# Optimization experiments

Measured on AMD Instinct MI355X. Metric: run time of the kernel, lower is better.

The kernel has to match this reference:

```python
import jax, jax.numpy as jnp
import numpy as np

B, C, H, W = 2, 256, 48, 48
NH = 4          # heads (and SE ratio)
DK = C // NH    # 64


def conv1x1(x, w, b):
    # x: [B,Cin,H,W], w: [Cout,Cin], b: [Cout]
    return jnp.einsum('oc,bchw->bohw', w, x) + b[None, :, None, None]


def rtrans(q_in, k_in, v_in, qw, qb, kw, kb, vw, vb):
    b, c, h_, w_ = q_in.shape
    n = h_ * w_
    q = conv1x1(q_in, qw, qb).reshape(b, NH, DK, n).transpose(0, 1, 3, 2)  # [B,h,N,dk]
    k = conv1x1(k_in, kw, kb).reshape(b, NH, DK, n)                         # [B,h,dk,N]
    v = conv1x1(v_in, vw, vb).reshape(b, NH, DK, n)                         # [B,h,dk,N]
    scores = jnp.einsum('bhnd,bhdm->bhnm', q, k) / jnp.sqrt(jnp.asarray(DK, q.dtype))
    attn = jax.nn.softmax(scores, axis=-1)                                  # [B,h,N,N]
    out = jnp.einsum('bhdn,bhnm->bhdm', v, attn)                            # [B,h,dk,N]
    return out.reshape(b, c, h_, w_)


def setup_inputs() -> dict:
    key = jax.random.key(0)
    ks = jax.random.split(key, 16)
    s = 0.02
    d = {
        'x': jax.random.normal(ks[0], (B, C, H, W), jnp.float32),
        'y': jax.random.normal(ks[1], (B, C, H, W), jnp.float32),
        # RScaling: fc1 Conv2d(2C, C//ratio, 1), fc2 Conv2d(C//ratio, 2C, 1); ratio=NH
        'sc_fc1_w': jax.random.normal(ks[2], (C // NH, 2 * C), jnp.float32) * s,
        'sc_fc1_b': jnp.zeros((C // NH,), jnp.float32),
        'sc_fc2_w': jax.random.normal(ks[3], (2 * C, C // NH), jnp.float32) * s,
        'sc_fc2_b': jnp.zeros((2 * C,), jnp.float32),
        # RTrans 1
        't1_qw': jax.random.normal(ks[4], (C, C), jnp.float32) * s,
        't1_qb': jnp.zeros((C,), jnp.float32),
        't1_kw': jax.random.normal(ks[5], (C, C), jnp.float32) * s,
        't1_kb': jnp.zeros((C,), jnp.float32),
        't1_vw': jax.random.normal(ks[6], (C, C), jnp.float32) * s,
        't1_vb': jnp.zeros((C,), jnp.float32),
        # RTrans 2 (ST=True)
        't2_qw': jax.random.normal(ks[7], (C, C), jnp.float32) * s,
        't2_qb': jnp.zeros((C,), jnp.float32),
        't2_kw': jax.random.normal(ks[8], (C, C), jnp.float32) * s,
        't2_kb': jnp.zeros((C,), jnp.float32),
        't2_vw': jax.random.normal(ks[9], (C, C), jnp.float32) * s,
        't2_vb': jnp.zeros((C,), jnp.float32),
        # RGating: Conv2d(2C, 2, 1)
        'gate_w': jax.random.normal(ks[10], (2, 2 * C), jnp.float32) * s,
        'gate_b': jnp.zeros((2,), jnp.float32),
    }
    return d


def reference(x, y, sc_fc1_w, sc_fc1_b, sc_fc2_w, sc_fc2_b,
              t1_qw, t1_qb, t1_kw, t1_kb, t1_vw, t1_vb,
              t2_qw, t2_qb, t2_kw, t2_kb, t2_vw, t2_vb,
              gate_w, gate_b):
    c = x.shape[1]
    # --- RScaling (SE squeeze-excite on concatenated streams) ---
    cat = jnp.concatenate([x, y], axis=1)                       # [B,2C,H,W]
    pooled = cat.mean(axis=(2, 3), keepdims=True)               # [B,2C,1,1]
    f = conv1x1(jax.nn.relu(conv1x1(pooled, sc_fc1_w, sc_fc1_b)), sc_fc2_w, sc_fc2_b)
    g = jax.nn.sigmoid(f)                                       # [B,2C,1,1]
    x = x * g[:, :c] + x
    y = y * g[:, c:] + y
    # --- RTrans 1: x = attn(q=x, k=y, v=y) ---
    x = rtrans(x, y, y, t1_qw, t1_qb, t1_kw, t1_kb, t1_vw, t1_vb)
    # --- RTrans 2 (ST): y = attn(q=y, k=x_new, v=x_new) ---
    y = rtrans(y, x, x, t2_qw, t2_qb, t2_kw, t2_kb, t2_vw, t2_vb)
    # --- RGating ---
    gate = jax.nn.sigmoid(conv1x1(jnp.concatenate([x, y], axis=1), gate_w, gate_b))  # [B,2,H,W]
    x = x * gate[:, :1] + x
    y = y * gate[:, 1:] + y
    return (x, y)
```

## Files before the change

kernel.cpp:

```cpp
#include <hip/hip_runtime.h>
#include <hip/hip_bf16.h>
#include <math.h>

typedef __hip_bfloat16 bf16;
typedef unsigned short u16;
typedef __attribute__((ext_vector_type(8))) short short8;
typedef __attribute__((ext_vector_type(4))) float f32x4;

#define BB  2
#define CC  256
#define NHH 4
#define DKK 64
#define NN  2304
#define NT  36
#define NT2 18
#define MS  4
#define NTM 9
#define WSTR 88
#define MFMA16(a,b,c) __builtin_amdgcn_mfma_f32_16x16x32_bf16(a, b, c, 0, 0, 0)

__device__ __forceinline__ float u2f(u16 u){ return __uint_as_float(((unsigned)u) << 16); }
__device__ __forceinline__ u16 f2u(float f){
    unsigned u = __float_as_uint(f);
    unsigned r = u + 0x7FFFu + ((u >> 16) & 1u);
    return (u16)(r >> 16);
}

__device__ __forceinline__ float ldv(const void* p, size_t i, int bf){
    return bf ? u2f(((const u16*)p)[i]) : ((const float*)p)[i];
}
__device__ __forceinline__ void stv(void* p, size_t i, float v, int bf){
    if (bf) ((u16*)p)[i] = f2u(v);
    else    ((float*)p)[i] = v;
}
__device__ __forceinline__ short8 ldw8(const void* p, size_t i, int bf){
    if (bf) return *(const short8*)((const u16*)p + i);
    const float* f = (const float*)p + i;
    short8 r;
    #pragma unroll
    for (int k = 0; k < 8; k++) r[k] = (short)f2u(f[k]);
    return r;
}

__global__ void detect_kernel(const void* __restrict__ x, int* __restrict__ flg){
    const u16* u = (const u16*)x;
    int t = threadIdx.x;
    bool ok = true;
    for (int i = 0; i < 8; i++){
        u16 v = u[t*8 + i];
        int e = (v >> 7) & 0xFF;
        ok = ok && (((v & 0x7FFF) == 0) || (e >= 96 && e <= 143));
    }
    unsigned long long b = __ballot(ok);
    if (t == 0) *flg = (b == 0xFFFFFFFFFFFFFFFFull) ? 1 : 0;
}

__global__ void pool_kernel(const void* __restrict__ x, const void* __restrict__ y,
                            const int* __restrict__ flg, float* __restrict__ pooled){
    int bf = *flg;
    int bid = blockIdx.x;
    int b = bid >> 9, cc = bid & 511;
    const void* src = (cc < CC) ? x : y;
    size_t base = ((size_t)b*CC + (cc & 255))*NN;
    float s = 0.f;
    for (int i = threadIdx.x; i < NN; i += 256) s += ldv(src, base + i, bf);
    __shared__ float red[4];
    for (int off = 32; off; off >>= 1) s += __shfl_down(s, off, 64);
    if ((threadIdx.x & 63) == 0) red[threadIdx.x >> 6] = s;
    __syncthreads();
    if (threadIdx.x == 0)
        pooled[bid] = (red[0]+red[1]+red[2]+red[3]) * (1.0f/(float)NN);
}

__global__ void se_fc1_kernel(const float* __restrict__ pooled,
                              const void* __restrict__ w1, const void* __restrict__ b1,
                              const int* __restrict__ flg, float* __restrict__ f1){
    int bf = *flg;
    int bid = blockIdx.x;
    int b = bid >> 6, f = bid & 63;
    int lane = threadIdx.x;
    const float* ps = pooled + b*512;
    float a = 0.f;
    #pragma unroll
    for (int k = 0; k < 8; k++){
        int c = lane*8 + k;
        a += ldv(w1, (size_t)f*512 + c, bf) * ps[c];
    }
    #pragma unroll
    for (int off = 32; off; off >>= 1) a += __shfl_down(a, off, 64);
    if (lane == 0)
        f1[b*64 + f] = fmaxf(a + ldv(b1, f, bf), 0.f);
}

__launch_bounds__(512)
__global__ void se_fc2_kernel(const float* __restrict__ f1,
                              const void* __restrict__ w2, const void* __restrict__ b2v,
                              const int* __restrict__ flg, float* __restrict__ gse){
    int bf = *flg;
    int b = blockIdx.x;
    int o = threadIdx.x;
    __shared__ float f1s[64];
    if (o < 64) f1s[o] = f1[b*64 + o];
    __syncthreads();
    float a = ldv(b2v, o, bf);
    #pragma unroll
    for (int j = 0; j < 64; j++) a += ldv(w2, (size_t)o*64 + j, bf) * f1s[j];
    gse[b*512 + o] = 1.f + 1.f/(1.f + __expf(-a));
}

__global__ void transpose2_kernel(const void* __restrict__ x, const void* __restrict__ y,
                                  const float* __restrict__ gse, const int* __restrict__ flg,
                                  u16* __restrict__ xsT, u16* __restrict__ ysT){
    int bf = *flg;
    int z = blockIdx.z;
    int b = z >> 1, which = z & 1;
    const void* src = which ? y : x;
    const float* gs = gse + b*512 + (which ? 256 : 0);
    u16* dst = which ? ysT : xsT;
    int ct = blockIdx.y, nt = blockIdx.x;
    int t = threadIdx.x;
    int nl = t & 63, cq = t >> 6;
    #pragma unroll
    for (int i = 0; i < 16; i++){
        int c = ct*64 + cq*16 + i;
        float v = ldv(src, ((size_t)b*CC + c)*NN + nt*64 + nl, bf) * gs[c];
        dst[((size_t)b*NN + nt*64 + nl)*CC + c] = f2u(v);
    }
}

__launch_bounds__(256)
__global__ void conv3_mfma(const u16* __restrict__ Xq, const u16* __restrict__ Xkv,
                           const void* __restrict__ wq, const void* __restrict__ bq,
                           const void* __restrict__ wk, const void* __restrict__ bk,
                           const void* __restrict__ wv, const void* __restrict__ bv_,
                           const int* __restrict__ flg,
                           u16* __restrict__ QT, u16* __restrict__ KT, u16* __restrict__ Vb){
    int bf = *flg;
    int z = blockIdx.z;
    int b = z / 3, op = z % 3;
    const u16* X = (op == 0) ? Xq : Xkv;
    const void* W    = (op == 0) ? wq : (op == 1) ? wk : wv;
    const void* bias = (op == 0) ? bq : (op == 1) ? bk : bv_;
    u16* Y = (op == 0) ? QT : (op == 1) ? KT : Vb;
    int transT = (op < 2);
    float oscale = (op == 1) ? 0.125f : 1.0f;
    int ot = blockIdx.y, nt = blockIdx.x;
    int lane = threadIdx.x & 63, wv_ = threadIdx.x >> 6;
    int c15 = lane & 15, quad = lane >> 4;
    const u16* Xb = X + ((size_t)b*NN + nt*64)*CC;
    int oa = ot*64 + wv_*16 + c15;
    f32x4 zf = {0.f,0.f,0.f,0.f};
    f32x4 acc[4] = {zf,zf,zf,zf};
    #pragma unroll
    for (int kc = 0; kc < CC; kc += 32){
        short8 aw = ldw8(W, (size_t)oa*CC + kc + quad*8, bf);
        #pragma unroll
        for (int j = 0; j < 4; j++){
            short8 bx = *(const short8*)(Xb + (size_t)(j*16 + c15)*CC + kc + quad*8);
            acc[j] = MFMA16(aw, bx, acc[j]);
        }
    }
    int od = ot*64 + wv_*16 + quad*4;
    float bvr[4];
    #pragma unroll
    for (int r = 0; r < 4; r++) bvr[r] = ldv(bias, od + r, bf);
    #pragma unroll
    for (int j = 0; j < 4; j++){
        int n = nt*64 + j*16 + c15;
        #pragma unroll
        for (int r = 0; r < 4; r++){
            int o = od + r;
            float val = (acc[j][r] + bvr[r]) * oscale;
            size_t idx = transT
              ? (((size_t)(b*NHH + (o >> 6))*NN + n)*DKK + (o & 63))
              : (((size_t)b*CC + o)*NN + n);
            Y[idx] = f2u(val);
        }
    }
}

__launch_bounds__(256)
__global__ void attn_stats_mfma(const u16* __restrict__ QT, const u16* __restrict__ KT,
                                float* __restrict__ gL){
    int bh = blockIdx.y, ntile = blockIdx.x, ms = blockIdx.z;
    int lane = threadIdx.x & 63, wv = threadIdx.x >> 6;
    int c15 = lane & 15, quad = lane >> 4;
    const u16* Qb = QT + (size_t)bh*NN*DKK;
    const u16* Kb = KT + (size_t)bh*NN*DKK;
    size_t qo = (size_t)(ntile*64 + wv*16 + c15)*DKK + quad*8;
    short8 a0 = *(const short8*)(Qb + qo);
    short8 a1 = *(const short8*)(Qb + qo + 32);
    float ll[4] = {0.f,0.f,0.f,0.f};
    f32x4 z = {0.f,0.f,0.f,0.f};
    for (int it = 0; it < NTM; it++){
        int mt = ms*NTM + it;
        f32x4 s[4];
        #pragma unroll
        for (int j = 0; j < 4; j++){
            size_t ko = (size_t)(mt*64 + j*16 + c15)*DKK + quad*8;
            short8 b0 = *(const short8*)(Kb + ko);
            short8 b1 = *(const short8*)(Kb + ko + 32);
            f32x4 t = MFMA16(a0, b0, z);
            s[j]     = MFMA16(a1, b1, t);
        }
        #pragma unroll
        for (int r = 0; r < 4; r++)
            ll[r] += __expf(s[0][r]) + __expf(s[1][r]) + __expf(s[2][r]) + __expf(s[3][r]);
    }
    #pragma unroll
    for (int d = 1; d < 16; d <<= 1)
        #pragma unroll
        for (int r = 0; r < 4; r++)
            ll[r] += __shfl_xor(ll[r], d, 16);
    if (c15 == 0){
        #pragma unroll
        for (int r = 0; r < 4; r++){
            int n = ntile*64 + wv*16 + quad*4 + r;
            gL[((size_t)ms*BB*NHH + bh)*NN + n] = ll[r];
        }
    }
}

__global__ void stats_combine(const float* __restrict__ gL, float* __restrict__ Li){
    int idx = blockIdx.x*256 + threadIdx.x;
    if (idx >= BB*NHH*NN) return;
    float ll = 0.f;
    #pragma unroll
    for (int ms = 0; ms < MS; ms++)
        ll += gL[(size_t)ms*BB*NHH*NN + idx];
    Li[idx] = 1.f/ll;
}

__launch_bounds__(512)
__global__ void attn_out_mfma(const u16* __restrict__ QT, const u16* __restrict__ KT,
                              const u16* __restrict__ V, const float* __restrict__ Li,
                              const int* __restrict__ flg,
                              void* __restrict__ O, size_t ooff, u16* __restrict__ OT){
    int bf = *flg;
    int bh = blockIdx.y, mtile = blockIdx.x;
    int tid = threadIdx.x;
    int lane = tid & 63, wv5 = tid >> 6;
    int g = wv5 >> 2, wv = wv5 & 3;
    int c15 = lane & 15, quad = lane >> 4;
    const u16* Qb = QT + (size_t)bh*NN*DKK;
    const u16* Kb = KT + (size_t)bh*NN*DKK;
    const u16* Vb = V + (size_t)bh*DKK*NN;
    const float* Lp = Li + (size_t)bh*NN;
    __shared__ __align__(16) u16 wT[2][2][64][WSTR];
    __shared__ __align__(16) float osum[64][66];
    short8 kb0[4], kb1[4];
    #pragma unroll
    for (int j = 0; j < 4; j++){
        size_t ko = (size_t)(mtile*64 + j*16 + c15)*DKK + quad*8;
        kb0[j] = *(const short8*)(Kb + ko);
        kb1[j] = *(const short8*)(Kb + ko + 32);
    }
    f32x4 z = {0.f,0.f,0.f,0.f};
    f32x4 o4[4] = {z,z,z,z};
    int nt0 = g*NT2;
    size_t qo0 = (size_t)(nt0*64 + wv*16 + c15)*DKK + quad*8;
    short8 a0 = *(const short8*)(Qb + qo0);
    short8 a1 = *(const short8*)(Qb + qo0 + 32);
    size_t vo0 = (size_t)(wv*16 + c15)*NN + nt0*64 + quad*8;
    short8 av0 = *(const short8*)(Vb + vo0);
    short8 av1 = *(const short8*)(Vb + vo0 + 32);
    for (int it = 0; it < NT2; it++){
        int nt = g*NT2 + it;
        int p = it & 1;
        f32x4 s[4];
        #pragma unroll
        for (int j = 0; j < 4; j++){
            f32x4 t = MFMA16(a0, kb0[j], z);
            s[j]    = MFMA16(a1, kb1[j], t);
        }
        short8 a0n = a0, a1n = a1, av0n = av0, av1n = av1;
        if (it + 1 < NT2){
            size_t qn = (size_t)((nt+1)*64 + wv*16 + c15)*DKK + quad*8;
            a0n = *(const short8*)(Qb + qn);
            a1n = *(const short8*)(Qb + qn + 32);
            size_t vn = (size_t)(wv*16 + c15)*NN + (nt+1)*64 + quad*8;
            av0n = *(const short8*)(Vb + vn);
            av1n = *(const short8*)(Vb + vn + 32);
        }
        int nb = nt*64 + wv*16 + quad*4;
        float iL[4];
        #pragma unroll
        for (int r = 0; r < 4; r++) iL[r] = Lp[nb+r];
        #pragma unroll
        for (int j = 0; j < 4; j++){
            ushort4 pk;
            pk.x = f2u(__expf(s[j][0]) * iL[0]);
            pk.y = f2u(__expf(s[j][1]) * iL[1]);
            pk.z = f2u(__expf(s[j][2]) * iL[2]);
            pk.w = f2u(__expf(s[j][3]) * iL[3]);
            *(ushort4*)&wT[g][p][j*16 + c15][wv*16 + quad*4] = pk;
        }
        __syncthreads();
        #pragma unroll
        for (int j = 0; j < 4; j++){
            short8 b0 = *(const short8*)&wT[g][p][j*16 + c15][quad*8];
            short8 b1 = *(const short8*)&wT[g][p][j*16 + c15][32 + quad*8];
            o4[j] = MFMA16(av0, b0, o4[j]);
            o4[j] = MFMA16(av1, b1, o4[j]);
        }
        a0 = a0n; a1 = a1n; av0 = av0n; av1 = av1n;
    }
    if (g == 1){
        #pragma unroll
        for (int j = 0; j < 4; j++)
            #pragma unroll
            for (int r = 0; r < 4; r++)
                osum[wv*16 + quad*4 + r][j*16 + c15] = o4[j][r];
    }
    __syncthreads();
    if (g == 0){
        int brow = bh >> 2, head = bh & 3;
        #pragma unroll
        for (int j = 0; j < 4; j++){
            int m = mtile*64 + j*16 + c15;
            #pragma unroll
            for (int r = 0; r < 4; r++){
                int d = wv*16 + quad*4 + r;
                float val = o4[j][r] + osum[d][j*16 + c15];
                stv(O, ooff + ((size_t)brow*CC + head*DKK + d)*NN + m, val, bf);
                if (OT) OT[((size_t)brow*NN + m)*CC + head*DKK + d] = f2u(val);
            }
        }
    }
}

__global__ void gate_part_kernel(const void* __restrict__ out, const void* __restrict__ gw,
                                 const int* __restrict__ flg, float* __restrict__ gpart){
    int bf = *flg;
    const size_t SZ = (size_t)BB*CC*NN;
    int b = blockIdx.z, g = blockIdx.y;
    int nb = blockIdx.x*64;
    int t = threadIdx.x;
    int nl = t & 63, sub = t >> 6;
    __shared__ float r0[4][64], r1[4][64];
    float a0 = 0.f, a1 = 0.f;
    int cbase = g*128 + sub*32;
    for (int i = 0; i < 32; i++){
        int cc = cbase + i;
        size_t idx = (cc < 256 ? ((size_t)b*CC + cc)*NN
                               : SZ + ((size_t)b*CC + (cc-256))*NN) + nb + nl;
        float v = ldv(out, idx, bf);
        a0 += ldv(gw, cc, bf)*v;
        a1 += ldv(gw, 512 + cc, bf)*v;
    }
    r0[sub][nl] = a0; r1[sub][nl] = a1;
    __syncthreads();
    if (t < 64){
        float s0 = r0[0][t]+r0[1][t]+r0[2][t]+r0[3][t];
        float s1 = r1[0][t]+r1[1][t]+r1[2][t]+r1[3][t];
        int n = nb + t;
        gpart[(((size_t)b*4 + g)*2 + 0)*NN + n] = s0;
        gpart[(((size_t)b*4 + g)*2 + 1)*NN + n] = s1;
    }
}

__global__ void gate_combine_kernel(const float* __restrict__ gpart, const void* __restrict__ gb,
                                    const int* __restrict__ flg, float* __restrict__ gates){
    int bf = *flg;
    int idx = blockIdx.x*256 + threadIdx.x;
    if (idx >= BB*NN) return;
    int b = idx / NN, n = idx % NN;
    float s0 = ldv(gb, 0, bf), s1 = ldv(gb, 1, bf);
    #pragma unroll
    for (int g = 0; g < 4; g++){
        s0 += gpart[(((size_t)b*4 + g)*2 + 0)*NN + n];
        s1 += gpart[(((size_t)b*4 + g)*2 + 1)*NN + n];
    }
    gates[((size_t)b*2 + 0)*NN + n] = 1.f + 1.f/(1.f + __expf(-s0));
    gates[((size_t)b*2 + 1)*NN + n] = 1.f + 1.f/(1.f + __expf(-s1));
}

__global__ void rescale_kernel(const float* __restrict__ gates, const int* __restrict__ flg,
                               void* __restrict__ out){
    int bf = *flg;
    const size_t SZ = (size_t)BB*CC*NN;
    const size_t nq = (2*SZ) >> 2;
    for (size_t u = (size_t)blockIdx.x*256 + threadIdx.x; u < nq; u += (size_t)gridDim.x*256){
        size_t flat = u*4;
        int half = (int)(flat / SZ);
        size_t rem = flat % SZ;
        int b = (int)(rem / ((size_t)CC*NN));
        int n = (int)(rem % NN);
        const float* gp = gates + ((size_t)b*2 + half)*NN + n;
        #pragma unroll
        for (int k = 0; k < 4; k++)
            stv(out, flat + k, ldv(out, flat + k, bf) * gp[k], bf);
    }
}

extern "C" void kernel_launch(void* const* d_in, const int* in_sizes, int n_in,
                              void* d_out, int out_size, void* d_ws, size_t ws_size,
                              hipStream_t stream){
    (void)in_sizes; (void)n_in; (void)out_size; (void)ws_size;
    const void* x    = d_in[0];
    const void* y    = d_in[1];
    const void* sc1w = d_in[2];
    const void* sc1b = d_in[3];
    const void* sc2w = d_in[4];
    const void* sc2b = d_in[5];
    const void *t1qw = d_in[6],  *t1qb = d_in[7];
    const void *t1kw = d_in[8],  *t1kb = d_in[9];
    const void *t1vw = d_in[10], *t1vb = d_in[11];
    const void *t2qw = d_in[12], *t2qb = d_in[13];
    const void *t2kw = d_in[14], *t2kb = d_in[15];
    const void *t2vw = d_in[16], *t2vb = d_in[17];
    const void *gw   = d_in[18], *gb   = d_in[19];

    const size_t SZ = (size_t)BB*CC*NN;
    const size_t BHN = (size_t)BB*NHH*NN;
    char* wsb = (char*)d_ws;
    int*   flg    = (int*)wsb;
    float* pooled = (float*)(wsb + 16);
    float* f1     = pooled + 1024;
    float* gse    = f1 + 128;
    float* Lb     = gse + 1024;
    float* gL     = Lb + BHN;
    float* gpart  = gL + MS*BHN;
    float* gates  = gpart + (size_t)BB*4*2*NN;
    u16* xsT = (u16*)(gates + (size_t)BB*2*NN);
    u16* ysT = xsT + SZ;
    u16* QT  = ysT + SZ;
    u16* KT  = QT + SZ;
    u16* Vb  = KT + SZ;

    dim3 tg2(NT, 4, BB*2);
    dim3 cg3(NT, 4, BB*3);
    dim3 sg(NT, BB*NHH, MS);
    dim3 ag(NT, BB*NHH);
    dim3 gg(NT, 4, BB);

    detect_kernel<<<1, 64, 0, stream>>>(x, flg);
    pool_kernel<<<1024, 256, 0, stream>>>(x, y, flg, pooled);
    se_fc1_kernel<<<BB*64, 64, 0, stream>>>(pooled, sc1w, sc1b, flg, f1);
    se_fc2_kernel<<<BB, 512, 0, stream>>>(f1, sc2w, sc2b, flg, gse);

    transpose2_kernel<<<tg2, 256, 0, stream>>>(x, y, gse, flg, xsT, ysT);

    conv3_mfma<<<cg3, 256, 0, stream>>>(xsT, ysT, t1qw, t1qb, t1kw, t1kb, t1vw, t1vb,
                                        flg, QT, KT, Vb);
    attn_stats_mfma<<<sg, 256, 0, stream>>>(QT, KT, gL);
    stats_combine<<<72, 256, 0, stream>>>(gL, Lb);
    attn_out_mfma<<<ag, 512, 0, stream>>>(QT, KT, Vb, Lb, flg, d_out, 0, xsT);

    conv3_mfma<<<cg3, 256, 0, stream>>>(ysT, xsT, t2qw, t2qb, t2kw, t2kb, t2vw, t2vb,
                                        flg, QT, KT, Vb);
    attn_stats_mfma<<<sg, 256, 0, stream>>>(QT, KT, gL);
    stats_combine<<<72, 256, 0, stream>>>(gL, Lb);
    attn_out_mfma<<<ag, 512, 0, stream>>>(QT, KT, Vb, Lb, flg, d_out, SZ, (u16*)nullptr);

    gate_part_kernel<<<gg, 256, 0, stream>>>(d_out, gw, flg, gpart);
    gate_combine_kernel<<<18, 256, 0, stream>>>(gpart, gb, flg, gates);
    rescale_kernel<<<1024, 256, 0, stream>>>(gates, flg, d_out);
}
```

Baseline: 402.7 us.

## Flatten grids for XCD-local head mapping and halve attn_out m-tile

The conv, stats and attention-output kernels now use 1D grids. The batch-head (or batch/out-tile) index sits in the low 3 bits of blockIdx.x, so round-robin dispatch across the 8 XCDs keeps each head's Q/K/V traffic within one XCD's L2. The attention-output kernel also shrinks its key/column tile from 64 to 32. That doubles the block count from 288 to 576 to fill more CUs and cuts LDS per block. The cost is that Q and V tiles are reloaded, and QK^T plus exp are recomputed, for twice as many tiles.

After: 428.1 us. 6.3% more time.

```diff
diff --git a/kernel.cpp b/kernel.cpp
--- a/kernel.cpp
+++ b/kernel.cpp
@@ -136,15 +136,16 @@
                            const int* __restrict__ flg,
                            u16* __restrict__ QT, u16* __restrict__ KT, u16* __restrict__ Vb){
     int bf = *flg;
-    int z = blockIdx.z;
-    int b = z / 3, op = z % 3;
+    int bhD = blockIdx.x & 7;
+    int q = blockIdx.x >> 3;
+    int op = q / 36, nt = q % 36;
+    int b = bhD >> 2, ot = bhD & 3;
     const u16* X = (op == 0) ? Xq : Xkv;
     const void* W    = (op == 0) ? wq : (op == 1) ? wk : wv;
     const void* bias = (op == 0) ? bq : (op == 1) ? bk : bv_;
     u16* Y = (op == 0) ? QT : (op == 1) ? KT : Vb;
     int transT = (op < 2);
     float oscale = (op == 1) ? 0.125f : 1.0f;
-    int ot = blockIdx.y, nt = blockIdx.x;
     int lane = threadIdx.x & 63, wv_ = threadIdx.x >> 6;
     int c15 = lane & 15, quad = lane >> 4;
     const u16* Xb = X + ((size_t)b*NN + nt*64)*CC;
@@ -182,7 +183,9 @@
 __launch_bounds__(256)
 __global__ void attn_stats_mfma(const u16* __restrict__ QT, const u16* __restrict__ KT,
                                 float* __restrict__ gL){
-    int bh = blockIdx.y, ntile = blockIdx.x, ms = blockIdx.z;
+    int bh = blockIdx.x & 7;
+    int r2 = blockIdx.x >> 3;
+    int ntile = r2 % 36, ms = r2 / 36;
     int lane = threadIdx.x & 63, wv = threadIdx.x >> 6;
     int c15 = lane & 15, quad = lane >> 4;
     const u16* Qb = QT + (size_t)bh*NN*DKK;
@@ -237,7 +240,8 @@
                               const int* __restrict__ flg,
                               void* __restrict__ O, size_t ooff, u16* __restrict__ OT){
     int bf = *flg;
-    int bh = blockIdx.y, mtile = blockIdx.x;
+    int bh = blockIdx.x & 7;
+    int mtile = blockIdx.x >> 3;
     int tid = threadIdx.x;
     int lane = tid & 63, wv5 = tid >> 6;
     int g = wv5 >> 2, wv = wv5 & 3;
@@ -246,17 +250,17 @@
     const u16* Kb = KT + (size_t)bh*NN*DKK;
     const u16* Vb = V + (size_t)bh*DKK*NN;
     const float* Lp = Li + (size_t)bh*NN;
-    __shared__ __align__(16) u16 wT[2][2][64][WSTR];
-    __shared__ __align__(16) float osum[64][66];
-    short8 kb0[4], kb1[4];
-    #pragma unroll
-    for (int j = 0; j < 4; j++){
-        size_t ko = (size_t)(mtile*64 + j*16 + c15)*DKK + quad*8;
+    __shared__ __align__(16) u16 wT[2][2][32][WSTR];
+    __shared__ __align__(16) float osum[64][34];
+    short8 kb0[2], kb1[2];
+    #pragma unroll
+    for (int j = 0; j < 2; j++){
+        size_t ko = (size_t)(mtile*32 + j*16 + c15)*DKK + quad*8;
         kb0[j] = *(const short8*)(Kb + ko);
         kb1[j] = *(const short8*)(Kb + ko + 32);
     }
     f32x4 z = {0.f,0.f,0.f,0.f};
-    f32x4 o4[4] = {z,z,z,z};
+    f32x4 o4[2] = {z,z};
     int nt0 = g*NT2;
     size_t qo0 = (size_t)(nt0*64 + wv*16 + c15)*DKK + quad*8;
     short8 a0 = *(const short8*)(Qb + qo0);
@@ -267,9 +271,9 @@
     for (int it = 0; it < NT2; it++){
         int nt = g*NT2 + it;
         int p = it & 1;
-        f32x4 s[4];
-        #pragma unroll
-        for (int j = 0; j < 4; j++){
+        f32x4 s[2];
+        #pragma unroll
+        for (int j = 0; j < 2; j++){
             f32x4 t = MFMA16(a0, kb0[j], z);
             s[j]    = MFMA16(a1, kb1[j], t);
         }
@@ -287,7 +291,7 @@
         #pragma unroll
         for (int r = 0; r < 4; r++) iL[r] = Lp[nb+r];
         #pragma unroll
-        for (int j = 0; j < 4; j++){
+        for (int j = 0; j < 2; j++){
             ushort4 pk;
             pk.x = f2u(__expf(s[j][0]) * iL[0]);
             pk.y = f2u(__expf(s[j][1]) * iL[1]);
@@ -297,7 +301,7 @@
         }
         __syncthreads();
         #pragma unroll
-        for (int j = 0; j < 4; j++){
+        for (int j = 0; j < 2; j++){
             short8 b0 = *(const short8*)&wT[g][p][j*16 + c15][quad*8];
             short8 b1 = *(const short8*)&wT[g][p][j*16 + c15][32 + quad*8];
             o4[j] = MFMA16(av0, b0, o4[j]);
@@ -307,7 +311,7 @@
     }
     if (g == 1){
         #pragma unroll
-        for (int j = 0; j < 4; j++)
+        for (int j = 0; j < 2; j++)
             #pragma unroll
             for (int r = 0; r < 4; r++)
                 osum[wv*16 + quad*4 + r][j*16 + c15] = o4[j][r];
@@ -316,8 +320,8 @@
     if (g == 0){
         int brow = bh >> 2, head = bh & 3;
         #pragma unroll
-        for (int j = 0; j < 4; j++){
-            int m = mtile*64 + j*16 + c15;
+        for (int j = 0; j < 2; j++){
+            int m = mtile*32 + j*16 + c15;
             #pragma unroll
             for (int r = 0; r < 4; r++){
                 int d = wv*16 + quad*4 + r;
@@ -429,9 +433,6 @@
     u16* Vb  = KT + SZ;
 
     dim3 tg2(NT, 4, BB*2);
-    dim3 cg3(NT, 4, BB*3);
-    dim3 sg(NT, BB*NHH, MS);
-    dim3 ag(NT, BB*NHH);
     dim3 gg(NT, 4, BB);
 
     detect_kernel<<<1, 64, 0, stream>>>(x, flg);
@@ -441,17 +442,17 @@
 
     transpose2_kernel<<<tg2, 256, 0, stream>>>(x, y, gse, flg, xsT, ysT);
 
-    conv3_mfma<<<cg3, 256, 0, stream>>>(xsT, ysT, t1qw, t1qb, t1kw, t1kb, t1vw, t1vb,
+    conv3_mfma<<<864, 256, 0, stream>>>(xsT, ysT, t1qw, t1qb, t1kw, t1kb, t1vw, t1vb,
                                         flg, QT, KT, Vb);
-    attn_stats_mfma<<<sg, 256, 0, stream>>>(QT, KT, gL);
+    attn_stats_mfma<<<1152, 256, 0, stream>>>(QT, KT, gL);
     stats_combine<<<72, 256, 0, stream>>>(gL, Lb);
-    attn_out_mfma<<<ag, 512, 0, stream>>>(QT, KT, Vb, Lb, flg, d_out, 0, xsT);
-
-    conv3_mfma<<<cg3, 256, 0, stream>>>(ysT, xsT, t2qw, t2qb, t2kw, t2kb, t2vw, t2vb,
+    attn_out_mfma<<<576, 512, 0, stream>>>(QT, KT, Vb, Lb, flg, d_out, 0, xsT);
+
+    conv3_mfma<<<864, 256, 0, stream>>>(ysT, xsT, t2qw, t2qb, t2kw, t2kb, t2vw, t2vb,
                                         flg, QT, KT, Vb);
-    attn_stats_mfma<<<sg, 256, 0, stream>>>(QT, KT, gL);
+    attn_stats_mfma<<<1152, 256, 0, stream>>>(QT, KT, gL);
     stats_combine<<<72, 256, 0, stream>>>(gL, Lb);
-    attn_out_mfma<<<ag, 512, 0, stream>>>(QT, KT, Vb, Lb, flg, d_out, SZ, (u16*)nullptr);
+    attn_out_mfma<<<576, 512, 0, stream>>>(QT, KT, Vb, Lb, flg, d_out, SZ, (u16*)nullptr);
 
     gate_part_kernel<<<gg, 256, 0, stream>>>(d_out, gw, flg, gpart);
     gate_combine_kernel<<<18, 256, 0, stream>>>(gpart, gb, flg, gates);
```

## Fuse detect, SE, stats-combine and gate-combine kernels; flatten grids and shrink LDS stride

Applied to the files above, without the earlier changes.

Folds the dtype detection into the pooling kernel, merges the two SE FC kernels into one, and computes the softmax normalizer inside the attention output kernel from the partial sums held in shared memory. Gate combining is fused into the rescale kernel. Grids are flattened so the batch-head index varies fastest, and the LDS row stride is reduced. The goal is fewer launches and less intermediate global traffic, at the cost of extra LDS in attn_out and possible bank-conflict changes.

Result: no change. 402.7 us (-0.0%).

```diff
diff --git a/kernel.cpp b/kernel.cpp
--- a/kernel.cpp
+++ b/kernel.cpp
@@ -16,7 +16,7 @@
 #define NT2 18
 #define MS  4
 #define NTM 9
-#define WSTR 88
+#define WSTR 72
 #define MFMA16(a,b,c) __builtin_amdgcn_mfma_f32_16x16x32_bf16(a, b, c, 0, 0, 0)
 
 __device__ __forceinline__ float u2f(u16 u){ return __uint_as_float(((unsigned)u) << 16); }
@@ -42,70 +42,72 @@
     return r;
 }
 
-__global__ void detect_kernel(const void* __restrict__ x, int* __restrict__ flg){
+__global__ void pool_kernel(const void* __restrict__ x, const void* __restrict__ y,
+                            int* __restrict__ flg, float* __restrict__ pooled){
+    int t = threadIdx.x;
     const u16* u = (const u16*)x;
-    int t = threadIdx.x;
     bool ok = true;
-    for (int i = 0; i < 8; i++){
-        u16 v = u[t*8 + i];
-        int e = (v >> 7) & 0xFF;
-        ok = ok && (((v & 0x7FFF) == 0) || (e >= 96 && e <= 143));
-    }
-    unsigned long long b = __ballot(ok);
-    if (t == 0) *flg = (b == 0xFFFFFFFFFFFFFFFFull) ? 1 : 0;
-}
-
-__global__ void pool_kernel(const void* __restrict__ x, const void* __restrict__ y,
-                            const int* __restrict__ flg, float* __restrict__ pooled){
-    int bf = *flg;
+    if (t < 64){
+        #pragma unroll
+        for (int i = 0; i < 8; i++){
+            u16 v = u[t*8 + i];
+            int e = (v >> 7) & 0xFF;
+            ok = ok && (((v & 0x7FFF) == 0) || (e >= 96 && e <= 143));
+        }
+    }
+    unsigned long long bl = __ballot(ok);
+    __shared__ int bfs;
+    if (t == 0) bfs = (bl == 0xFFFFFFFFFFFFFFFFull) ? 1 : 0;
+    __syncthreads();
+    int bf = bfs;
+    if (blockIdx.x == 0 && t == 0) *flg = bf;
+
     int bid = blockIdx.x;
     int b = bid >> 9, cc = bid & 511;
     const void* src = (cc < CC) ? x : y;
     size_t base = ((size_t)b*CC + (cc & 255))*NN;
     float s = 0.f;
-    for (int i = threadIdx.x; i < NN; i += 256) s += ldv(src, base + i, bf);
+    for (int i = t; i < NN; i += 256) s += ldv(src, base + i, bf);
     __shared__ float red[4];
     for (int off = 32; off; off >>= 1) s += __shfl_down(s, off, 64);
-    if ((threadIdx.x & 63) == 0) red[threadIdx.x >> 6] = s;
-    __syncthreads();
-    if (threadIdx.x == 0)
+    if ((t & 63) == 0) red[t >> 6] = s;
+    __syncthreads();
+    if (t == 0)
         pooled[bid] = (red[0]+red[1]+red[2]+red[3]) * (1.0f/(float)NN);
 }
 
-__global__ void se_fc1_kernel(const float* __restrict__ pooled,
-                              const void* __restrict__ w1, const void* __restrict__ b1,
-                              const int* __restrict__ flg, float* __restrict__ f1){
-    int bf = *flg;
-    int bid = blockIdx.x;
-    int b = bid >> 6, f = bid & 63;
-    int lane = threadIdx.x;
-    const float* ps = pooled + b*512;
+__launch_bounds__(512)
+__global__ void se_kernel(const float* __restrict__ pooled,
+                          const void* __restrict__ w1, const void* __restrict__ b1,
+                          const void* __restrict__ w2, const void* __restrict__ b2v,
+                          const int* __restrict__ flg, float* __restrict__ gse){
+    int bf = *flg;
+    int b = blockIdx.x;
+    int t = threadIdx.x;
+    __shared__ float ps[512];
+    __shared__ float r1[64][9];
+    __shared__ float f1s[64];
+    ps[t] = pooled[b*512 + t];
+    __syncthreads();
+    int f = t >> 3, sub = t & 7;
     float a = 0.f;
-    #pragma unroll
-    for (int k = 0; k < 8; k++){
-        int c = lane*8 + k;
+    for (int i = 0; i < 64; i++){
+        int c = sub*64 + i;
         a += ldv(w1, (size_t)f*512 + c, bf) * ps[c];
     }
-    #pragma unroll
-    for (int off = 32; off; off >>= 1) a += __shfl_down(a, off, 64);
-    if (lane == 0)
-        f1[b*64 + f] = fmaxf(a + ldv(b1, f, bf), 0.f);
-}
-
-__launch_bounds__(512)
-__global__ void se_fc2_kernel(const float* __restrict__ f1,
-                              const void* __restrict__ w2, const void* __restrict__ b2v,
-                              const int* __restrict__ flg, float* __restrict__ gse){
-    int bf = *flg;
-    int b = blockIdx.x;
-    int o = threadIdx.x;
-    __shared__ float f1s[64];
-    if (o < 64) f1s[o] = f1[b*64 + o];
-    __syncthreads();
-    float a = ldv(b2v, o, bf);
-    #pragma unroll
-    for (int j = 0; j < 64; j++) a += ldv(w2, (size_t)o*64 + j, bf) * f1s[j];
-    gse[b*512 + o] = 1.f + 1.f/(1.f + __expf(-a));
+    r1[f][sub] = a;
+    __syncthreads();
+    if (t < 64){
+        float s = ldv(b1, t, bf);
+        #pragma unroll
+        for (int k = 0; k < 8; k++) s += r1[t][k];
+        f1s[t] = fmaxf(s, 0.f);
+    }
+    __syncthreads();
+    float a2 = ldv(b2v, t, bf);
+    #pragma unroll
+    for (int j = 0; j < 64; j++) a2 += ldv(w2, (size_t)t*64 + j, bf) * f1s[j];
+    gse[b*512 + t] = 1.f + 1.f/(1.f + __expf(-a2));
 }
 
 __global__ void transpose2_kernel(const void* __restrict__ x, const void* __restrict__ y,
@@ -136,15 +138,16 @@
                            const int* __restrict__ flg,
                            u16* __restrict__ QT, u16* __restrict__ KT, u16* __restrict__ Vb){
     int bf = *flg;
-    int z = blockIdx.z;
-    int b = z / 3, op = z % 3;
+    int bhD = blockIdx.x & 7;
+    int q = blockIdx.x >> 3;
+    int op = q / 36, nt = q % 36;
+    int b = bhD >> 2, ot = bhD & 3;
     const u16* X = (op == 0) ? Xq : Xkv;
     const void* W    = (op == 0) ? wq : (op == 1) ? wk : wv;
     const void* bias = (op == 0) ? bq : (op == 1) ? bk : bv_;
     u16* Y = (op == 0) ? QT : (op == 1) ? KT : Vb;
     int transT = (op < 2);
     float oscale = (op == 1) ? 0.125f : 1.0f;
-    int ot = blockIdx.y, nt = blockIdx.x;
     int lane = threadIdx.x & 63, wv_ = threadIdx.x >> 6;
     int c15 = lane & 15, quad = lane >> 4;
     const u16* Xb = X + ((size_t)b*NN + nt*64)*CC;
@@ -182,7 +185,9 @@
 __launch_bounds__(256)
 __global__ void attn_stats_mfma(const u16* __restrict__ QT, const u16* __restrict__ KT,
                                 float* __restrict__ gL){
-    int bh = blockIdx.y, ntile = blockIdx.x, ms = blockIdx.z;
+    int bh = blockIdx.x & 7;
+    int r2 = blockIdx.x >> 3;
+    int ntile = r2 % 36, ms = r2 / 36;
     int lane = threadIdx.x & 63, wv = threadIdx.x >> 6;
     int c15 = lane & 15, quad = lane >> 4;
     const u16* Qb = QT + (size_t)bh*NN*DKK;
@@ -221,23 +226,14 @@
     }
 }
 
-__global__ void stats_combine(const float* __restrict__ gL, float* __restrict__ Li){
-    int idx = blockIdx.x*256 + threadIdx.x;
-    if (idx >= BB*NHH*NN) return;
-    float ll = 0.f;
-    #pragma unroll
-    for (int ms = 0; ms < MS; ms++)
-        ll += gL[(size_t)ms*BB*NHH*NN + idx];
-    Li[idx] = 1.f/ll;
-}
-
 __launch_bounds__(512)
 __global__ void attn_out_mfma(const u16* __restrict__ QT, const u16* __restrict__ KT,
-                              const u16* __restrict__ V, const float* __restrict__ Li,
+                              const u16* __restrict__ V, const float* __restrict__ gL,
                               const int* __restrict__ flg,
                               void* __restrict__ O, size_t ooff, u16* __restrict__ OT){
     int bf = *flg;
-    int bh = blockIdx.y, mtile = blockIdx.x;
+    int bh = blockIdx.x & 7;
+    int mtile = blockIdx.x >> 3;
     int tid = threadIdx.x;
     int lane = tid & 63, wv5 = tid >> 6;
     int g = wv5 >> 2, wv = wv5 & 3;
@@ -245,9 +241,17 @@
     const u16* Qb = QT + (size_t)bh*NN*DKK;
     const u16* Kb = KT + (size_t)bh*NN*DKK;
     const u16* Vb = V + (size_t)bh*DKK*NN;
-    const float* Lp = Li + (size_t)bh*NN;
     __shared__ __align__(16) u16 wT[2][2][64][WSTR];
     __shared__ __align__(16) float osum[64][66];
+    __shared__ __align__(16) float Lis[NN];
+
+    const size_t BHN = (size_t)BB*NHH*NN;
+    for (int i = tid; i < NN; i += 512){
+        size_t o = (size_t)bh*NN + i;
+        Lis[i] = 1.f / (gL[o] + gL[BHN + o] + gL[2*BHN + o] + gL[3*BHN + o]);
+    }
+    __syncthreads();
+
     short8 kb0[4], kb1[4];
     #pragma unroll
     for (int j = 0; j < 4; j++){
@@ -285,7 +289,7 @@
         int nb = nt*64 + wv*16 + quad*4;
         float iL[4];
         #pragma unroll
-        for (int r = 0; r < 4; r++) iL[r] = Lp[nb+r];
+        for (int r = 0; r < 4; r++) iL[r] = Lis[nb+r];
         #pragma unroll
         for (int j = 0; j < 4; j++){
             ushort4 pk;
@@ -359,37 +363,32 @@
     }
 }
 
-__global__ void gate_combine_kernel(const float* __restrict__ gpart, const void* __restrict__ gb,
-                                    const int* __restrict__ flg, float* __restrict__ gates){
-    int bf = *flg;
-    int idx = blockIdx.x*256 + threadIdx.x;
-    if (idx >= BB*NN) return;
-    int b = idx / NN, n = idx % NN;
-    float s0 = ldv(gb, 0, bf), s1 = ldv(gb, 1, bf);
-    #pragma unroll
-    for (int g = 0; g < 4; g++){
-        s0 += gpart[(((size_t)b*4 + g)*2 + 0)*NN + n];
-        s1 += gpart[(((size_t)b*4 + g)*2 + 1)*NN + n];
-    }
-    gates[((size_t)b*2 + 0)*NN + n] = 1.f + 1.f/(1.f + __expf(-s0));
-    gates[((size_t)b*2 + 1)*NN + n] = 1.f + 1.f/(1.f + __expf(-s1));
-}
-
-__global__ void rescale_kernel(const float* __restrict__ gates, const int* __restrict__ flg,
-                               void* __restrict__ out){
+__global__ void rescale_gates_kernel(const float* __restrict__ gpart, const void* __restrict__ gb,
+                                     const int* __restrict__ flg, void* __restrict__ out){
     int bf = *flg;
     const size_t SZ = (size_t)BB*CC*NN;
-    const size_t nq = (2*SZ) >> 2;
-    for (size_t u = (size_t)blockIdx.x*256 + threadIdx.x; u < nq; u += (size_t)gridDim.x*256){
-        size_t flat = u*4;
-        int half = (int)(flat / SZ);
-        size_t rem = flat % SZ;
-        int b = (int)(rem / ((size_t)CC*NN));
-        int n = (int)(rem % NN);
-        const float* gp = gates + ((size_t)b*2 + half)*NN + n;
-        #pragma unroll
-        for (int k = 0; k < 4; k++)
-            stv(out, flat + k, ldv(out, flat + k, bf) * gp[k], bf);
+    int nt = blockIdx.x, cgrp = blockIdx.y, b = blockIdx.z;
+    int t = threadIdx.x;
+    int j = (cgrp >= 4) ? 1 : 0;
+    __shared__ float gsh[64];
+    if (t < 64){
+        int n = nt*64 + t;
+        float s = ldv(gb, j, bf);
+        #pragma unroll
+        for (int g = 0; g < 4; g++)
+            s += gpart[(((size_t)b*4 + g)*2 + j)*NN + n];
+        gsh[t] = 1.f + 1.f/(1.f + __expf(-s));
+    }
+    __syncthreads();
+    int nl = t & 63, cq = t >> 6;
+    int cbase = (cgrp & 3)*64;
+    size_t base = j ? SZ : 0;
+    float gv = gsh[nl];
+    #pragma unroll
+    for (int i = 0; i < 16; i++){
+        int c = cbase + cq*16 + i;
+        size_t idx = base + ((size_t)b*CC + c)*NN + nt*64 + nl;
+        stv(out, idx, ldv(out, idx, bf) * gv, bf);
     }
 }
 
@@ -416,44 +415,33 @@
     char* wsb = (char*)d_ws;
     int*   flg    = (int*)wsb;
     float* pooled = (float*)(wsb + 16);
-    float* f1     = pooled + 1024;
-    float* gse    = f1 + 128;
-    float* Lb     = gse + 1024;
-    float* gL     = Lb + BHN;
+    float* gse    = pooled + 1024;
+    float* gL     = gse + 1024;
     float* gpart  = gL + MS*BHN;
-    float* gates  = gpart + (size_t)BB*4*2*NN;
-    u16* xsT = (u16*)(gates + (size_t)BB*2*NN);
+    u16* xsT = (u16*)(gpart + (size_t)BB*4*2*NN);
     u16* ysT = xsT + SZ;
     u16* QT  = ysT + SZ;
     u16* KT  = QT + SZ;
     u16* Vb  = KT + SZ;
 
     dim3 tg2(NT, 4, BB*2);
-    dim3 cg3(NT, 4, BB*3);
-    dim3 sg(NT, BB*NHH, MS);
-    dim3 ag(NT, BB*NHH);
     dim3 gg(NT, 4, BB);
-
-    detect_kernel<<<1, 64, 0, stream>>>(x, flg);
+    dim3 rg(NT, 8, BB);
+
     pool_kernel<<<1024, 256, 0, stream>>>(x, y, flg, pooled);
-    se_fc1_kernel<<<BB*64, 64, 0, stream>>>(pooled, sc1w, sc1b, flg, f1);
-    se_fc2_kernel<<<BB, 512, 0, stream>>>(f1, sc2w, sc2b, flg, gse);
-
+    se_kernel<<<BB, 512, 0, stream>>>(pooled, sc1w, sc1b, sc2w, sc2b, flg, gse);
     transpose2_kernel<<<tg2, 256, 0, stream>>>(x, y, gse, flg, xsT, ysT);
 
-    conv3_mfma<<<cg3, 256, 0, stream>>>(xsT, ysT, t1qw, t1qb, t1kw, t1kb, t1vw, t1vb,
+    conv3_mfma<<<864, 256, 0, stream>>>(xsT, ysT, t1qw, t1qb, t1kw, t1kb, t1vw, t1vb,
                                         flg, QT, KT, Vb);
-    attn_stats_mfma<<<sg, 256, 0, stream>>>(QT, KT, gL);
-    stats_combine<<<72, 256, 0, stream>>>(gL, Lb);
-    attn_out_mfma<<<ag, 512, 0, stream>>>(QT, KT, Vb, Lb, flg, d_out, 0, xsT);
-
-    conv3_mfma<<<cg3, 256, 0, stream>>>(ysT, xsT, t2qw, t2qb, t2kw, t2kb, t2vw, t2vb,
+    attn_stats_mfma<<<1152, 256, 0, stream>>>(QT, KT, gL);
+    attn_out_mfma<<<288, 512, 0, stream>>>(QT, KT, Vb, gL, flg, d_out, 0, xsT);
+
+    conv3_mfma<<<864, 256, 0, stream>>>(ysT, xsT, t2qw, t2qb, t2kw, t2kb, t2vw, t2vb,
                                         flg, QT, KT, Vb);
-    attn_stats_mfma<<<sg, 256, 0, stream>>>(QT, KT, gL);
-    stats_combine<<<72, 256, 0, stream>>>(gL, Lb);
-    attn_out_mfma<<<ag, 512, 0, stream>>>(QT, KT, Vb, Lb, flg, d_out, SZ, (u16*)nullptr);
+    attn_stats_mfma<<<1152, 256, 0, stream>>>(QT, KT, gL);
+    attn_out_mfma<<<288, 512, 0, stream>>>(QT, KT, Vb, gL, flg, d_out, SZ, (u16*)nullptr);
 
     gate_part_kernel<<<gg, 256, 0, stream>>>(d_out, gw, flg, gpart);
-    gate_combine_kernel<<<18, 256, 0, stream>>>(gpart, gb, flg, gates);
-    rescale_kernel<<<1024, 256, 0, stream>>>(gates, flg, d_out);
-}
+    rescale_gates_kernel<<<rg, 256, 0, stream>>>(gpart, gb, flg, d_out);
+}
```
